# Kernel tuning notes

Measured on AMD Instinct MI355X. Metric: run time of the kernel, lower is better.

The kernel has to match this reference:

```python
import jax, jax.numpy as jnp
import numpy as np

B, N, D = 8, 2048, 256      # batch, tokens, model dim (= out_token_dims)
S = 128                     # query_key_dims
H = int(2.0 * D)            # expansion_factor * D = 512
EPS = 1e-5


def setup_inputs() -> dict:
    key = jax.random.key(0)
    ks = jax.random.split(key, 4)
    x = jax.random.normal(ks[0], (B, N, D), dtype=jnp.float32)
    g = jnp.ones((), jnp.float32)                                # ScaleNorm gain
    W_uv = jax.random.normal(ks[1], (D, 2 * H + S), jnp.float32) * 0.02
    b_uv = jnp.zeros((2 * H + S,), jnp.float32)
    gamma = jnp.ones((2, S), jnp.float32)                        # OffsetScale scale
    beta = jnp.zeros((2, S), jnp.float32)                        # OffsetScale offset
    W_o = jax.random.normal(ks[2], (H, D), jnp.float32) * 0.02
    b_o = jnp.zeros((D,), jnp.float32)
    return {"x": x, "g": g, "W_uv": W_uv, "b_uv": b_uv,
            "gamma": gamma, "beta": beta, "W_o": W_o, "b_o": b_o}


def reference(x, g, W_uv, b_uv, gamma, beta, W_o, b_o):
    d = x.shape[-1]
    # ScaleNorm: x / max(||x|| / sqrt(d), eps) * g
    norm = jnp.linalg.norm(x, axis=-1, keepdims=True) * jax.lax.rsqrt(jnp.float32(d))
    xn = x / jnp.maximum(norm, EPS) * g
    # fused uv projection + SiLU
    uv = jax.nn.silu(jnp.einsum('bnd,de->bne', xn, W_uv) + b_uv)
    u = uv[..., :H]            # gate branch        [B,N,H]
    v = uv[..., H:2 * H]       # value branch       [B,N,H]
    base = uv[..., 2 * H:]     # shared q/k base    [B,N,S]
    # OffsetScale heads=2 -> q, k (cheap per-dim affine)
    q = base * gamma[0] + beta[0]
    k = base * gamma[1] + beta[1]
    # single-head scores + ReLU^2 attention activation
    qk = jnp.einsum('bns,bms->bnm', q, k) * jax.lax.rsqrt(jnp.float32(S))
    attn = jnp.square(jax.nn.relu(qk))
    # gate * (attn @ v), then output projection back to D
    gated = u * jnp.einsum('bnm,bmh->bnh', attn, v)
    return jnp.einsum('bnh,hd->bnd', gated, W_o) + b_o
```

## Files before the change

### kernel.cpp

```cpp
#include <hip/hip_runtime.h>
#include <math.h>

#define BB 8
#define NN 2048
#define DD 256
#define SS 128
#define HH 512
#define EE 1152

typedef short bf16x8 __attribute__((ext_vector_type(8)));
typedef float f32x4 __attribute__((ext_vector_type(4)));

__device__ __forceinline__ short f2bf(float f) {
    union { float f; unsigned u; } a; a.f = f;
    unsigned r = a.u + 0x7FFFu + ((a.u >> 16) & 1u);
    return (short)(r >> 16);
}
__device__ __forceinline__ float bf2f(short s) {
    union { unsigned u; float f; } a; a.u = ((unsigned)(unsigned short)s) << 16;
    return a.f;
}
__device__ __forceinline__ void gl_lds16(const short* g, short* l) {
    __builtin_amdgcn_global_load_lds(
        (const __attribute__((address_space(1))) void*)g,
        (__attribute__((address_space(3))) void*)l, 16, 0, 0);
}

__global__ __launch_bounds__(256) void k_pre(
        const float* __restrict__ x, const float* __restrict__ gp,
        short* __restrict__ xn,
        const float* __restrict__ Wuv, const float* __restrict__ Wo,
        short* __restrict__ Wuv_t, short* __restrict__ Wo_t) {
    __shared__ float tile[32][33];
    int bid = blockIdx.x;
    int t = threadIdx.x;
    if (bid < 4096) {
        int wave = t >> 6, lane = t & 63;
        long row = (long)bid * 4 + wave;
        float4 xv = ((const float4*)(x + row * DD))[lane];
        float ss = xv.x*xv.x + xv.y*xv.y + xv.z*xv.z + xv.w*xv.w;
        #pragma unroll
        for (int off = 32; off > 0; off >>= 1) ss += __shfl_down(ss, off);
        ss = __shfl(ss, 0);
        float norm = sqrtf(ss) * 0.0625f;
        float scale = gp[0] / fmaxf(norm, 1e-5f);
        short4 o;
        o.x = f2bf(xv.x * scale); o.y = f2bf(xv.y * scale);
        o.z = f2bf(xv.z * scale); o.w = f2bf(xv.w * scale);
        ((short4*)(xn + row * DD))[lane] = o;
    } else if (bid < 4384) {
        int bid2 = bid - 4096;
        int et = bid2 % 36, dt = bid2 / 36;
        #pragma unroll
        for (int i = 0; i < 4; i++) {
            int idx = t + i*256, r = idx >> 5, c = idx & 31;
            tile[r][c] = Wuv[(long)(dt*32 + r)*EE + et*32 + c];
        }
        __syncthreads();
        #pragma unroll
        for (int i = 0; i < 4; i++) {
            int idx = t + i*256, r = idx >> 5, c = idx & 31;
            Wuv_t[(long)(et*32 + r)*DD + dt*32 + c] = f2bf(tile[c][r]);
        }
    } else {
        int bid3 = bid - 4384;
        int ht = bid3 % 16, dt = bid3 / 16;
        #pragma unroll
        for (int i = 0; i < 4; i++) {
            int idx = t + i*256, r = idx >> 5, c = idx & 31;
            tile[r][c] = Wo[(long)(ht*32 + r)*DD + dt*32 + c];
        }
        __syncthreads();
        #pragma unroll
        for (int i = 0; i < 4; i++) {
            int idx = t + i*256, r = idx >> 5, c = idx & 31;
            Wo_t[(long)(dt*32 + r)*HH + ht*32 + c] = f2bf(tile[c][r]);
        }
    }
}

#define GOFF(row,cbb) ((((row)>>1)*64) + \
    (((((row)&1)*64 + (cbb)) ^ ((((row)>>1)&7)<<4)) >> 1))

__global__ __launch_bounds__(256, 3) void k_gemm1(
        const short* __restrict__ xn, const short* __restrict__ Wuv_t,
        const float* __restrict__ b_uv,
        const float* __restrict__ gamma, const float* __restrict__ beta,
        short* __restrict__ u, short* __restrict__ vfrag,
        short* __restrict__ q, short* __restrict__ k) {
    __shared__ short As[3][128*32];
    __shared__ short Bs[3][128*32];
    int m0 = blockIdx.x * 128, n0 = blockIdx.y * 128;
    int t = threadIdx.x, w = t >> 6, lane = t & 63;
    int wr = w & 1, wc = w >> 1, l16 = lane & 15, quad = lane >> 4;
    int sql  = (((lane & 7) ^ (lane >> 3)) * 16);
    int srow = ((lane >> 3) * 2) + (sql >> 6);
    int scb  = (sql & 63) >> 1;
    f32x4 acc[4][4] = {};
    #pragma unroll
    for (int ps = 0; ps < 2; ps++) {
        #pragma unroll
        for (int i = 0; i < 2; i++) {
            int r0 = i*64 + w*16;
            gl_lds16(&xn[(long)(m0 + r0 + srow)*DD + ps*32 + scb], &As[ps][r0*32]);
            gl_lds16(&Wuv_t[(long)(n0 + r0 + srow)*DD + ps*32 + scb], &Bs[ps][r0*32]);
        }
    }
    for (int ks = 0; ks < 8; ks++) {
        int cur = ks - (ks/3)*3;
        if (ks < 7) asm volatile("s_waitcnt vmcnt(4)" ::: "memory");
        else        asm volatile("s_waitcnt vmcnt(0)" ::: "memory");
        __builtin_amdgcn_s_barrier();
        if (ks + 2 < 8) {
            int nb = (ks+2) - ((ks+2)/3)*3;
            int k0 = (ks+2)*32;
            #pragma unroll
            for (int i = 0; i < 2; i++) {
                int r0 = i*64 + w*16;
                gl_lds16(&xn[(long)(m0 + r0 + srow)*DD + k0 + scb], &As[nb][r0*32]);
                gl_lds16(&Wuv_t[(long)(n0 + r0 + srow)*DD + k0 + scb], &Bs[nb][r0*32]);
            }
        }
        bf16x8 a[4], bb[4];
        #pragma unroll
        for (int mt = 0; mt < 4; mt++)
            a[mt] = *(const bf16x8*)&As[cur][GOFF(wr*64 + mt*16 + l16, quad*16)];
        #pragma unroll
        for (int nt = 0; nt < 4; nt++)
            bb[nt] = *(const bf16x8*)&Bs[cur][GOFF(wc*64 + nt*16 + l16, quad*16)];
        #pragma unroll
        for (int mt = 0; mt < 4; mt++)
            #pragma unroll
            for (int nt = 0; nt < 4; nt++)
                acc[mt][nt] = __builtin_amdgcn_mfma_f32_16x16x32_bf16(
                    a[mt], bb[nt], acc[mt][nt], 0,0,0);
    }
    #pragma unroll
    for (int mt = 0; mt < 4; mt++)
    #pragma unroll
    for (int nt = 0; nt < 4; nt++) {
        int gm0 = m0 + wr*64 + mt*16 + quad*4;
        int ge  = n0 + wc*64 + nt*16 + l16;
        float val[4];
        #pragma unroll
        for (int r = 0; r < 4; r++) {
            float xv = acc[mt][nt][r] + b_uv[ge];
            val[r] = xv / (1.0f + __expf(-xv));
        }
        if (ge < HH) {
            #pragma unroll
            for (int r = 0; r < 4; r++)
                u[(long)(gm0 + r)*HH + ge] = f2bf(val[r]);
        } else if (ge < 2*HH) {
            int h = ge - HH;
            long base = (((long)((gm0 >> 11)*64 + ((gm0 & 2047) >> 5)) * 32)
                         + (h >> 4)) * 512
                        + ((((gm0 & 31) >> 3)*16 + (h & 15)) * 8) + (gm0 & 7);
            short4 o;
            o.x = f2bf(val[0]); o.y = f2bf(val[1]);
            o.z = f2bf(val[2]); o.w = f2bf(val[3]);
            *(short4*)&vfrag[base] = o;
        } else {
            int si = ge - 2*HH;
            #pragma unroll
            for (int r = 0; r < 4; r++) {
                q[(long)(gm0 + r)*SS + si] = f2bf(val[r] * gamma[si]      + beta[si]);
                k[(long)(gm0 + r)*SS + si] = f2bf(val[r] * gamma[SS + si] + beta[SS + si]);
            }
        }
    }
}

#define KSW(pp,row,cb) (smem + ((pp)*64 + (row))*128 + \
    ((((cb) ^ (((row)&15)<<4))) >> 1))
#define PSW(pp,row,cb) (smem + 16384 + ((pp)*64 + (row))*64 + \
    ((((cb) ^ (((row)&7)<<4))) >> 1))
#define GTW(row,cb)    (smem + (row)*512 + ((((cb) ^ (((row)&15)<<4))) >> 1))

__global__ __launch_bounds__(1024, 4) void k_attn(
        const short* __restrict__ q, const short* __restrict__ k,
        const short* __restrict__ vfrag, const short* __restrict__ u,
        const short* __restrict__ Wo_t, const float* __restrict__ b_o,
        float* __restrict__ out) {
    extern __shared__ __align__(16) short smem[];
    int b = blockIdx.x & 7;
    int i0 = (blockIdx.x >> 3) * 64;
    int t = threadIdx.x, w = t >> 6, lane = t & 63;
    int l16 = lane & 15, quad = lane >> 4;
    int qt = w >> 2, mtile = w & 3;
    const short* qb  = q + ((long)b * NN + i0) * SS;
    const short* kb  = k + (long)b * NN * SS;
    const short* vfb = vfrag + (long)b * 64 * 32 * 512;
    const float RS = 0.08838834764831845f;

    int krow = t >> 4, kch = t & 15;

    bf16x8 qf[4];
    #pragma unroll
    for (int kc = 0; kc < 4; kc++)
        qf[kc] = *(const bf16x8*)&qb[(long)(qt*16 + l16)*SS + kc*32 + quad*8];

    *(bf16x8*)KSW(0, krow, kch*16) = *(const bf16x8*)&kb[(long)krow*SS + kch*8];
    bf16x8 kpre = *(const bf16x8*)&kb[(long)(64 + krow)*SS + kch*8];
    __syncthreads();

    f32x4 acc[4][2] = {};
    for (int it = 0; it < NN/64; it++) {
        int p = it & 1;
        int m0 = it * 64;
        int mnext = (m0 + 128 < NN) ? m0 + 128 : m0;
        bf16x8 knext = *(const bf16x8*)&kb[(long)(mnext + krow)*SS + kch*8];
        bf16x8 vf[2][2];
        #pragma unroll
        for (int s = 0; s < 2; s++)
            #pragma unroll
            for (int j = 0; j < 2; j++)
                vf[s][j] = *(const bf16x8*)
                    &vfb[((long)(it*2 + s)*32 + (w*2 + j))*512 + lane*8];
        f32x4 sc = {};
        #pragma unroll
        for (int kc = 0; kc < 4; kc++) {
            bf16x8 kf = *(const bf16x8*)KSW(p, mtile*16 + l16, kc*64 + quad*16);
            sc = __builtin_amdgcn_mfma_f32_16x16x32_bf16(kf, qf[kc], sc, 0,0,0);
        }
        short4 pw;
        {
            float s0 = fmaxf(sc[0]*RS, 0.f), s1 = fmaxf(sc[1]*RS, 0.f);
            float s2 = fmaxf(sc[2]*RS, 0.f), s3 = fmaxf(sc[3]*RS, 0.f);
            pw.x = f2bf(s0*s0); pw.y = f2bf(s1*s1);
            pw.z = f2bf(s2*s2); pw.w = f2bf(s3*s3);
        }
        *(short4*)PSW(p, qt*16 + l16, mtile*32 + quad*8) = pw;
        *(bf16x8*)KSW(p^1, krow, kch*16) = kpre;
        kpre = knext;
        __syncthreads();
        __builtin_amdgcn_s_setprio(1);
        #pragma unroll
        for (int s = 0; s < 2; s++) {
            bf16x8 af[4];
            #pragma unroll
            for (int qq = 0; qq < 4; qq++)
                af[qq] = *(const bf16x8*)PSW(p, qq*16 + l16, s*64 + quad*16);
            #pragma unroll
            for (int qq = 0; qq < 4; qq++)
                #pragma unroll
                for (int j = 0; j < 2; j++)
                    acc[qq][j] = __builtin_amdgcn_mfma_f32_16x16x32_bf16(
                        af[qq], vf[s][j], acc[qq][j], 0,0,0);
        }
        __builtin_amdgcn_s_setprio(0);
    }

    long rowbase = (long)b * NN + i0;
    __syncthreads();
    #pragma unroll
    for (int qq = 0; qq < 4; qq++)
    #pragma unroll
    for (int j = 0; j < 2; j++) {
        int gh = w*32 + j*16 + l16;
        #pragma unroll
        for (int r = 0; r < 4; r++) {
            int row = qq*16 + quad*4 + r;
            float uval = bf2f(u[(rowbase + row)*HH + gh]);
            *GTW(row, 2*gh) = f2bf(acc[qq][j][r] * uval);
        }
    }
    __syncthreads();
    f32x4 acc2[4] = {};
    #pragma unroll
    for (int kc = 0; kc < 16; kc++) {
        bf16x8 A[4];
        #pragma unroll
        for (int qq = 0; qq < 4; qq++)
            A[qq] = *(const bf16x8*)GTW(qq*16 + l16, kc*64 + quad*16);
        bf16x8 Bf = *(const bf16x8*)&Wo_t[(long)(w*16 + l16)*HH + kc*32 + quad*8];
        #pragma unroll
        for (int qq = 0; qq < 4; qq++)
            acc2[qq] = __builtin_amdgcn_mfma_f32_16x16x32_bf16(A[qq], Bf, acc2[qq], 0,0,0);
    }
    #pragma unroll
    for (int qq = 0; qq < 4; qq++)
    #pragma unroll
    for (int r = 0; r < 4; r++) {
        long grow = rowbase + qq*16 + quad*4 + r;
        int gd = w*16 + l16;
        out[grow*DD + gd] = acc2[qq][r] + b_o[gd];
    }
}

extern "C" void kernel_launch(void* const* d_in, const int* in_sizes, int n_in,
                              void* d_out, int out_size, void* d_ws, size_t ws_size,
                              hipStream_t stream) {
    const float* x     = (const float*)d_in[0];
    const float* g     = (const float*)d_in[1];
    const float* Wuv   = (const float*)d_in[2];
    const float* b_uv  = (const float*)d_in[3];
    const float* gamma = (const float*)d_in[4];
    const float* beta  = (const float*)d_in[5];
    const float* Wo    = (const float*)d_in[6];
    const float* b_o   = (const float*)d_in[7];
    float* out = (float*)d_out;

    short* ws    = (short*)d_ws;
    short* xn    = ws;
    short* Wuv_t = xn    + (long)16384 * 256;
    short* Wo_t  = Wuv_t + (long)1152 * 256;
    short* u     = Wo_t  + (long)256 * 512;
    short* vfrag = u     + (long)16384 * 512;
    short* qq    = vfrag + (long)16384 * 512;
    short* kk    = qq    + (long)16384 * 128;

    k_pre<<<4512, 256, 0, stream>>>(x, g, xn, Wuv, Wo, Wuv_t, Wo_t);
    k_gemm1<<<dim3(128, 9), 256, 0, stream>>>(xn, Wuv_t, b_uv, gamma, beta,
                                              u, vfrag, qq, kk);
    k_attn<<<256, 1024, 65536, stream>>>(qq, kk, vfrag, u, Wo_t, b_o, out);
}
```

Baseline: 166.3 us.

## Load gemm1 MFMA fragments directly from global memory, dropping LDS staging

```diff
diff --git a/kernel.cpp b/kernel.cpp
--- a/kernel.cpp
+++ b/kernel.cpp
@@ -79,55 +79,27 @@
     }
 }
 
-#define GOFF(row,cbb) ((((row)>>1)*64) + \
-    (((((row)&1)*64 + (cbb)) ^ ((((row)>>1)&7)<<4)) >> 1))
-
 __global__ __launch_bounds__(256, 3) void k_gemm1(
         const short* __restrict__ xn, const short* __restrict__ Wuv_t,
         const float* __restrict__ b_uv,
         const float* __restrict__ gamma, const float* __restrict__ beta,
         short* __restrict__ u, short* __restrict__ vfrag,
         short* __restrict__ q, short* __restrict__ k) {
-    __shared__ short As[3][128*32];
-    __shared__ short Bs[3][128*32];
     int m0 = blockIdx.x * 128, n0 = blockIdx.y * 128;
     int t = threadIdx.x, w = t >> 6, lane = t & 63;
     int wr = w & 1, wc = w >> 1, l16 = lane & 15, quad = lane >> 4;
-    int sql  = (((lane & 7) ^ (lane >> 3)) * 16);
-    int srow = ((lane >> 3) * 2) + (sql >> 6);
-    int scb  = (sql & 63) >> 1;
+    const short* Ab = xn    + (long)(m0 + wr*64 + l16)*DD + quad*8;
+    const short* Bb = Wuv_t + (long)(n0 + wc*64 + l16)*DD + quad*8;
     f32x4 acc[4][4] = {};
     #pragma unroll
-    for (int ps = 0; ps < 2; ps++) {
-        #pragma unroll
-        for (int i = 0; i < 2; i++) {
-            int r0 = i*64 + w*16;
-            gl_lds16(&xn[(long)(m0 + r0 + srow)*DD + ps*32 + scb], &As[ps][r0*32]);
-            gl_lds16(&Wuv_t[(long)(n0 + r0 + srow)*DD + ps*32 + scb], &Bs[ps][r0*32]);
-        }
-    }
     for (int ks = 0; ks < 8; ks++) {
-        int cur = ks - (ks/3)*3;
-        if (ks < 7) asm volatile("s_waitcnt vmcnt(4)" ::: "memory");
-        else        asm volatile("s_waitcnt vmcnt(0)" ::: "memory");
-        __builtin_amdgcn_s_barrier();
-        if (ks + 2 < 8) {
-            int nb = (ks+2) - ((ks+2)/3)*3;
-            int k0 = (ks+2)*32;
-            #pragma unroll
-            for (int i = 0; i < 2; i++) {
-                int r0 = i*64 + w*16;
-                gl_lds16(&xn[(long)(m0 + r0 + srow)*DD + k0 + scb], &As[nb][r0*32]);
-                gl_lds16(&Wuv_t[(long)(n0 + r0 + srow)*DD + k0 + scb], &Bs[nb][r0*32]);
-            }
-        }
         bf16x8 a[4], bb[4];
         #pragma unroll
         for (int mt = 0; mt < 4; mt++)
-            a[mt] = *(const bf16x8*)&As[cur][GOFF(wr*64 + mt*16 + l16, quad*16)];
+            a[mt] = *(const bf16x8*)&Ab[mt*16*DD + ks*32];
         #pragma unroll
         for (int nt = 0; nt < 4; nt++)
-            bb[nt] = *(const bf16x8*)&Bs[cur][GOFF(wc*64 + nt*16 + l16, quad*16)];
+            bb[nt] = *(const bf16x8*)&Bb[nt*16*DD + ks*32];
         #pragma unroll
         for (int mt = 0; mt < 4; mt++)
             #pragma unroll
```

New measurement: 183.9 us. 1.11x slower.
